# Performance work log

Measured on AMD Instinct MI355X. Metric: run time of the kernel, lower is better.

Reference implementation:

```python
import jax, jax.numpy as jnp
import numpy as np

# Config constants (from DeepSeekConfig / init_kwargs)
NUM_EXPERTS = 6
VAR_EXPERTS = 4
FIXED_EXPERTS = NUM_EXPERTS - VAR_EXPERTS  # 2
TOP_K = 2
D_MODEL = 1024
D_FF = 4 * D_MODEL
LN_EPS = 1e-5


def setup_inputs() -> dict:
    key = jax.random.key(0)
    ks = jax.random.split(key, 6)
    B, S = 2, 2048
    x = jax.random.normal(ks[0], (B, S, D_MODEL), dtype=jnp.float32)
    router_W = jax.random.normal(ks[1], (D_MODEL, VAR_EXPERTS), dtype=jnp.float32) * 0.02
    # stacked expert FFN params: (E, D, 4D) and (E, 4D, D)
    W1 = jax.random.normal(ks[2], (NUM_EXPERTS, D_MODEL, D_FF), dtype=jnp.float32) * 0.02
    b1 = jnp.zeros((NUM_EXPERTS, D_FF), dtype=jnp.float32)
    W2 = jax.random.normal(ks[3], (NUM_EXPERTS, D_FF, D_MODEL), dtype=jnp.float32) * 0.02
    b2 = jnp.zeros((NUM_EXPERTS, D_MODEL), dtype=jnp.float32)
    ln_gamma = jnp.ones((D_MODEL,), dtype=jnp.float32)
    ln_beta = jnp.zeros((D_MODEL,), dtype=jnp.float32)
    return {"x": x, "router_W": router_W, "W1": W1, "b1": b1, "W2": W2,
            "b2": b2, "ln_gamma": ln_gamma, "ln_beta": ln_beta}


def reference(x, router_W, W1, b1, W2, b2, ln_gamma, ln_beta):
    B, S, D = x.shape
    # router over the VARIABLE experts only
    router_logits = jnp.einsum('bsd,de->bse', x, router_W)          # (B,S,VAR)
    router_probs = jax.nn.softmax(router_logits, axis=-1)
    _, topk_idx = jax.lax.top_k(router_probs, TOP_K)                 # (B,S,K)
    adj_idx = topk_idx + FIXED_EXPERTS                               # global expert ids in [FIXED, NUM)

    # dense per-expert FFN on all tokens: experts[e](x) = gelu(x@W1[e]+b1[e]) @ W2[e] + b2[e]
    h = jnp.einsum('bsd,edf->ebsf', x, W1) + b1[:, None, None, :]    # (E,B,S,4D)
    h = jax.nn.gelu(h, approximate=False)                            # torch F.gelu default = exact
    all_out = jnp.einsum('ebsf,efd->ebsd', h, W2) + b2[:, None, None, :]  # (E,B,S,D)

    # fixed experts: all of experts[0:FIXED] applied to every token
    fixed_sum = all_out[:FIXED_EXPERTS].sum(axis=0)                  # (B,S,D)

    # variable experts: per-token gather of the top-k selected experts
    b_ix = jnp.arange(B)[:, None, None]
    s_ix = jnp.arange(S)[None, :, None]
    var = all_out[adj_idx, b_ix, s_ix, :]                            # (B,S,K,D)

    # cat along expert slot dim then mean == sum / (FIXED + K); topk probs unused (plain mean)
    combined = (fixed_sum + var.sum(axis=2)) / (FIXED_EXPERTS + TOP_K)

    # LayerNorm (biased variance, eps=1e-5)
    mu = combined.mean(axis=-1, keepdims=True)
    v = combined.var(axis=-1, keepdims=True)
    out = (combined - mu) / jnp.sqrt(v + LN_EPS) * ln_gamma + ln_beta
    return out, router_logits
```

## Files before the change

kernel.cpp:

```cpp
#include <hip/hip_runtime.h>
#include <cstdint>
#include <cstddef>

#define D_MODEL 1024
#define D_FF 4096
#define NTOK 4096
#define LN_EPS 1e-5f

typedef __bf16 bf16x8 __attribute__((ext_vector_type(8)));
typedef float f32x4 __attribute__((ext_vector_type(4)));
typedef unsigned short u16x4 __attribute__((ext_vector_type(4)));
typedef unsigned short u16x8 __attribute__((ext_vector_type(8)));

static __device__ __forceinline__ unsigned short f2bf(float f) {
    union { float f; unsigned u; } v; v.f = f;
    unsigned r = v.u + 0x7fffu + ((v.u >> 16) & 1u);
    return (unsigned short)(r >> 16);
}

static __device__ __forceinline__ float gelu_fast(float x) {
    float x2 = x * x;
    float a = x * __builtin_fmaf(-0.0713548162726f, x2, -1.59576912161f);
    float e = __expf(a);
    return x * __builtin_amdgcn_rcpf(1.0f + e);
}

static __device__ __forceinline__ void gload16(const void* g, void* l) {
    __builtin_amdgcn_global_load_lds(
        (const __attribute__((address_space(1))) void*)g,
        (__attribute__((address_space(3))) void*)l, 16, 0, 0);
}

static __device__ __forceinline__ void seg_of(const int* cnt, int seg[4], int pc[4]) {
    int o = 2 * NTOK;
    #pragma unroll
    for (int e = 0; e < 4; ++e) {
        int c = cnt[e * 32];
        pc[e] = (c + 127) & ~127;
        seg[e] = o;
        o += pc[e];
    }
}

__global__ __launch_bounds__(256) void convx_kernel(const float* __restrict__ x,
                                                    unsigned short* __restrict__ xb) {
    int idx = blockIdx.x * 256 + threadIdx.x;
    f32x4 v = *(const f32x4*)&x[(size_t)idx * 4];
    u16x4 b;
    b[0] = f2bf(v[0]); b[1] = f2bf(v[1]); b[2] = f2bf(v[2]); b[3] = f2bf(v[3]);
    *(u16x4*)&xb[(size_t)idx * 4] = b;
}

__global__ __launch_bounds__(256) void transpose_kernel(const float* __restrict__ W,
                                                        unsigned short* __restrict__ Wt,
                                                        int K, int N) {
    __shared__ unsigned short t[64][65];
    int k0 = blockIdx.y * 64, n0 = blockIdx.x * 64;
    const float* We = W + (size_t)blockIdx.z * K * N;
    unsigned short* Wte = Wt + (size_t)blockIdx.z * K * N;
    #pragma unroll
    for (int i = 0; i < 4; ++i) {
        int idx = threadIdx.x + i * 256;
        int kr = idx >> 4, c4 = idx & 15;
        f32x4 v = *(const f32x4*)&We[(size_t)(k0 + kr) * N + n0 + c4 * 4];
        #pragma unroll
        for (int j = 0; j < 4; ++j) t[c4 * 4 + j][kr] = f2bf(v[j]);
    }
    __syncthreads();
    #pragma unroll
    for (int i = 0; i < 2; ++i) {
        int idx = threadIdx.x + i * 256;
        int nr = idx >> 3, ck = idx & 7;
        u16x8 w;
        #pragma unroll
        for (int j = 0; j < 8; ++j) w[j] = t[nr][ck * 8 + j];
        *(u16x8*)&Wte[(size_t)(n0 + nr) * K + k0 + ck * 8] = w;
    }
}

__global__ __launch_bounds__(256) void router_kernel(
        const float* __restrict__ x, const float* __restrict__ rW,
        float* __restrict__ logits, int* __restrict__ selpk,
        int* __restrict__ slotpk, int* __restrict__ cnt, int* __restrict__ list) {
    __shared__ int se[8];
    __shared__ int sslot[8];
    int wid = threadIdx.x >> 6, lane = threadIdx.x & 63;
    int t = blockIdx.x * 4 + wid;
    const float* xr = x + (size_t)t * D_MODEL;
    float a0 = 0.f, a1 = 0.f, a2 = 0.f, a3 = 0.f;
    for (int d = lane; d < D_MODEL; d += 64) {
        float xv = xr[d];
        const float* w = rW + d * 4;
        a0 += xv * w[0]; a1 += xv * w[1]; a2 += xv * w[2]; a3 += xv * w[3];
    }
    #pragma unroll
    for (int off = 32; off; off >>= 1) {
        a0 += __shfl_xor(a0, off); a1 += __shfl_xor(a1, off);
        a2 += __shfl_xor(a2, off); a3 += __shfl_xor(a3, off);
    }
    if (lane == 0) {
        float l[4] = {a0, a1, a2, a3};
        logits[t * 4 + 0] = a0; logits[t * 4 + 1] = a1;
        logits[t * 4 + 2] = a2; logits[t * 4 + 3] = a3;
        int e0 = 0; float b = l[0];
        #pragma unroll
        for (int e = 1; e < 4; ++e) if (l[e] > b) { b = l[e]; e0 = e; }
        int e1 = -1; float b2 = -1e30f;
        #pragma unroll
        for (int e = 0; e < 4; ++e) {
            if (e == e0) continue;
            if (l[e] > b2) { b2 = l[e]; e1 = e; }
        }
        se[wid * 2] = e0; se[wid * 2 + 1] = e1;
    }
    __syncthreads();
    if (threadIdx.x == 0) {
        int cnts[4] = {0, 0, 0, 0}, base[4];
        #pragma unroll
        for (int k = 0; k < 8; ++k) cnts[se[k]]++;
        #pragma unroll
        for (int e = 0; e < 4; ++e)
            if (cnts[e]) base[e] = atomicAdd(&cnt[e * 32], cnts[e]);
        int run[4] = {0, 0, 0, 0};
        #pragma unroll
        for (int k = 0; k < 8; ++k) {
            int e = se[k];
            int s = base[e] + run[e]++;
            sslot[k] = s;
            list[e * NTOK + s] = blockIdx.x * 4 + (k >> 1);
        }
    }
    __syncthreads();
    if (lane == 0) {
        selpk[t] = se[wid * 2] | (se[wid * 2 + 1] << 8);
        slotpk[t] = sslot[wid * 2] | (sslot[wid * 2 + 1] << 16);
    }
}

__global__ __launch_bounds__(256) void pass1_kernel(
        const unsigned short* __restrict__ xb, const unsigned short* __restrict__ W1t,
        const float* __restrict__ b1, unsigned short* __restrict__ h,
        const int* __restrict__ cnt, const int* __restrict__ list, int fc, int BF) {
    __shared__ unsigned short As[128 * 64];
    __shared__ unsigned short Bs[128 * 64];
    const int e = blockIdx.z;
    const int tid = threadIdx.x, lane = tid & 63, wid = tid >> 6;
    int ecnt = NTOK, rowbase;
    if (e < 2) {
        rowbase = e * NTOK + blockIdx.y * 128;
    } else {
        int seg[4], pc[4];
        seg_of(cnt, seg, pc);
        int ev = e - 2;
        ecnt = cnt[ev * 32];
        if ((int)blockIdx.y * 128 >= pc[ev]) return;
        rowbase = seg[ev] + blockIdx.y * 128;
    }
    const int n0 = blockIdx.x * 128;

    const unsigned short* asrc[4];
    const unsigned short* bsrc[4];
    const unsigned short* W1e = W1t + (size_t)e * D_FF * D_MODEL;
    #pragma unroll
    for (int j = 0; j < 4; ++j) {
        int row = (wid * 4 + j) * 8 + (lane >> 3);
        int kc = lane & 7;
        int tok;
        if (e < 2) tok = blockIdx.y * 128 + row;
        else {
            int s = blockIdx.y * 128 + row;
            tok = (s < ecnt) ? list[(e - 2) * NTOK + s] : 0;
        }
        asrc[j] = xb + (size_t)tok * D_MODEL + ((kc ^ (row & 7)) << 3);
        bsrc[j] = W1e + (size_t)(fc + n0 + row) * D_MODEL + ((kc ^ (row & 7)) << 3);
    }
    const int wm = (wid >> 1) * 64, wn = (wid & 1) * 64;

    f32x4 acc[4][4];
    #pragma unroll
    for (int i = 0; i < 4; ++i)
        #pragma unroll
        for (int j = 0; j < 4; ++j) acc[i][j] = (f32x4)0.f;

    for (int kb = 0; kb < D_MODEL; kb += 64) {
        #pragma unroll
        for (int j = 0; j < 4; ++j) gload16(asrc[j] + kb, &As[(wid * 4 + j) * 512]);
        #pragma unroll
        for (int j = 0; j < 4; ++j) gload16(bsrc[j] + kb, &Bs[(wid * 4 + j) * 512]);
        asm volatile("s_waitcnt vmcnt(0)" ::: "memory");
        __syncthreads();
        #pragma unroll
        for (int kk = 0; kk < 2; ++kk) {
            int kof = kk * 32 + (lane >> 4) * 8;
            bf16x8 a[4], b[4];
            #pragma unroll
            for (int mi = 0; mi < 4; ++mi) {
                int r = wm + mi * 16 + (lane & 15);
                a[mi] = *(const bf16x8*)&As[r * 64 + (kof ^ ((r & 7) << 3))];
            }
            #pragma unroll
            for (int ni = 0; ni < 4; ++ni) {
                int r = wn + ni * 16 + (lane & 15);
                b[ni] = *(const bf16x8*)&Bs[r * 64 + (kof ^ ((r & 7) << 3))];
            }
            #pragma unroll
            for (int mi = 0; mi < 4; ++mi)
                #pragma unroll
                for (int ni = 0; ni < 4; ++ni)
                    acc[mi][ni] = __builtin_amdgcn_mfma_f32_16x16x32_bf16(
                        a[mi], b[ni], acc[mi][ni], 0, 0, 0);
        }
        __syncthreads();
    }

    const float* b1e = b1 + (size_t)e * D_FF + fc + n0;
    #pragma unroll
    for (int ni = 0; ni < 4; ++ni) {
        int col = wn + ni * 16 + (lane & 15);
        float bias = b1e[col];
        #pragma unroll
        for (int mi = 0; mi < 4; ++mi) {
            #pragma unroll
            for (int j = 0; j < 4; ++j) {
                int row = wm + mi * 16 + (lane >> 4) * 4 + j;
                float v = acc[mi][ni][j] + bias;
                h[(size_t)(rowbase + row) * BF + n0 + col] = f2bf(gelu_fast(v));
            }
        }
    }
}

__global__ __launch_bounds__(256) void pass2_kernel(
        const unsigned short* __restrict__ h, const unsigned short* __restrict__ W2t,
        const float* __restrict__ b2, float* __restrict__ oslab,
        const int* __restrict__ cnt, int fc, int BF, int first) {
    __shared__ unsigned short As[128 * 64];
    __shared__ unsigned short Bs[128 * 64];
    const int e = blockIdx.z;
    const int tid = threadIdx.x, lane = tid & 63, wid = tid >> 6;
    int rowbase;
    if (e < 2) {
        rowbase = e * NTOK + blockIdx.y * 128;
    } else {
        int seg[4], pc[4];
        seg_of(cnt, seg, pc);
        int ev = e - 2;
        if ((int)blockIdx.y * 128 >= pc[ev]) return;
        rowbase = seg[ev] + blockIdx.y * 128;
    }
    const int n0 = blockIdx.x * 128;

    const unsigned short* asrc[4];
    const unsigned short* bsrc[4];
    const unsigned short* W2e = W2t + (size_t)e * D_MODEL * D_FF;
    #pragma unroll
    for (int j = 0; j < 4; ++j) {
        int row = (wid * 4 + j) * 8 + (lane >> 3);
        int kc = lane & 7;
        asrc[j] = h + (size_t)(rowbase + row) * BF + ((kc ^ (row & 7)) << 3);
        bsrc[j] = W2e + (size_t)(n0 + row) * D_FF + fc + ((kc ^ (row & 7)) << 3);
    }
    const int wm = (wid >> 1) * 64, wn = (wid & 1) * 64;

    f32x4 acc[4][4];
    #pragma unroll
    for (int i = 0; i < 4; ++i)
        #pragma unroll
        for (int j = 0; j < 4; ++j) acc[i][j] = (f32x4)0.f;

    for (int kb = 0; kb < BF; kb += 64) {
        #pragma unroll
        for (int j = 0; j < 4; ++j) gload16(asrc[j] + kb, &As[(wid * 4 + j) * 512]);
        #pragma unroll
        for (int j = 0; j < 4; ++j) gload16(bsrc[j] + kb, &Bs[(wid * 4 + j) * 512]);
        asm volatile("s_waitcnt vmcnt(0)" ::: "memory");
        __syncthreads();
        #pragma unroll
        for (int kk = 0; kk < 2; ++kk) {
            int kof = kk * 32 + (lane >> 4) * 8;
            bf16x8 a[4], b[4];
            #pragma unroll
            for (int mi = 0; mi < 4; ++mi) {
                int r = wm + mi * 16 + (lane & 15);
                a[mi] = *(const bf16x8*)&As[r * 64 + (kof ^ ((r & 7) << 3))];
            }
            #pragma unroll
            for (int ni = 0; ni < 4; ++ni) {
                int r = wn + ni * 16 + (lane & 15);
                b[ni] = *(const bf16x8*)&Bs[r * 64 + (kof ^ ((r & 7) << 3))];
            }
            #pragma unroll
            for (int mi = 0; mi < 4; ++mi)
                #pragma unroll
                for (int ni = 0; ni < 4; ++ni)
                    acc[mi][ni] = __builtin_amdgcn_mfma_f32_16x16x32_bf16(
                        a[mi], b[ni], acc[mi][ni], 0, 0, 0);
        }
        __syncthreads();
    }

    const float* b2e = b2 + (size_t)e * D_MODEL + n0;
    #pragma unroll
    for (int ni = 0; ni < 4; ++ni) {
        int col = wn + ni * 16 + (lane & 15);
        float bias = first ? b2e[col] : 0.f;
        #pragma unroll
        for (int mi = 0; mi < 4; ++mi) {
            #pragma unroll
            for (int j = 0; j < 4; ++j) {
                int row = wm + mi * 16 + (lane >> 4) * 4 + j;
                size_t idx = (size_t)(rowbase + row) * D_MODEL + n0 + col;
                float v = acc[mi][ni][j] + bias;
                if (first) oslab[idx] = v;
                else       oslab[idx] += v;
            }
        }
    }
}

__global__ __launch_bounds__(256) void pass3_kernel(
        const float* __restrict__ oslab, const int* __restrict__ selpk,
        const int* __restrict__ slotpk, const int* __restrict__ cnt,
        const float* __restrict__ gamma, const float* __restrict__ beta,
        float* __restrict__ out) {
    int t = blockIdx.x;
    int seg[4], pc[4];
    seg_of(cnt, seg, pc);
    int sp = selpk[t], sl = slotpk[t];
    int e0 = sp & 0xff, e1 = (sp >> 8) & 0xff;
    int s0 = sl & 0xffff, s1 = (sl >> 16) & 0xffff;
    const float* p0 = oslab + (size_t)t * D_MODEL;
    const float* p1 = oslab + (size_t)(NTOK + t) * D_MODEL;
    const float* p2 = oslab + (size_t)(seg[e0] + s0) * D_MODEL;
    const float* p3 = oslab + (size_t)(seg[e1] + s1) * D_MODEL;
    float c[4];
    float sum = 0.f, sq = 0.f;
    #pragma unroll
    for (int i = 0; i < 4; ++i) {
        int d = threadIdx.x + i * 256;
        float v = (p0[d] + p1[d] + p2[d] + p3[d]) * 0.25f;
        c[i] = v; sum += v; sq += v * v;
    }
    #pragma unroll
    for (int off = 32; off; off >>= 1) {
        sum += __shfl_xor(sum, off);
        sq  += __shfl_xor(sq, off);
    }
    __shared__ float red[8];
    int lane = threadIdx.x & 63, wid = threadIdx.x >> 6;
    if (lane == 0) { red[wid] = sum; red[4 + wid] = sq; }
    __syncthreads();
    sum = red[0] + red[1] + red[2] + red[3];
    sq  = red[4] + red[5] + red[6] + red[7];
    float mean = sum * (1.0f / 1024.0f);
    float var = sq * (1.0f / 1024.0f) - mean * mean;
    float inv = rsqrtf(var + LN_EPS);
    #pragma unroll
    for (int i = 0; i < 4; ++i) {
        int d = threadIdx.x + i * 256;
        out[(size_t)t * D_MODEL + d] = (c[i] - mean) * inv * gamma[d] + beta[d];
    }
}

extern "C" void kernel_launch(void* const* d_in, const int* in_sizes, int n_in,
                              void* d_out, int out_size, void* d_ws, size_t ws_size,
                              hipStream_t stream) {
    const float* x   = (const float*)d_in[0];
    const float* rW  = (const float*)d_in[1];
    const float* W1  = (const float*)d_in[2];
    const float* b1  = (const float*)d_in[3];
    const float* W2  = (const float*)d_in[4];
    const float* b2  = (const float*)d_in[5];
    const float* gam = (const float*)d_in[6];
    const float* bet = (const float*)d_in[7];
    float* out = (float*)d_out;
    float* logits = out + (size_t)NTOK * D_MODEL;

    char* ws = (char*)d_ws;
    int* cnt    = (int*)ws;
    int* selpk  = (int*)(ws + 0x1000);
    int* slotpk = (int*)(ws + 0x6000);
    int* list   = (int*)(ws + 0xB000);
    unsigned short* xb  = (unsigned short*)(ws + 0x20000);
    unsigned short* W1t = (unsigned short*)(ws + 0x820000);
    unsigned short* W2t = (unsigned short*)(ws + 0x3820000);
    float* oslab        = (float*)(ws + 0x6820000);
    const size_t h_off  = 0x6820000 + (size_t)16896 * D_MODEL * 4;
    unsigned short* h   = (unsigned short*)(ws + h_off);

    int BF = 1024;
    for (int cand = 4096; cand >= 1024; cand >>= 1) {
        size_t need = h_off + (size_t)16896 * cand * 2;
        if (need <= ws_size) { BF = cand; break; }
    }

    convx_kernel<<<NTOK * D_MODEL / 4 / 256, 256, 0, stream>>>(x, xb);
    transpose_kernel<<<dim3(D_FF / 64, D_MODEL / 64, 6), 256, 0, stream>>>(W1, W1t, D_MODEL, D_FF);
    transpose_kernel<<<dim3(D_MODEL / 64, D_FF / 64, 6), 256, 0, stream>>>(W2, W2t, D_FF, D_MODEL);
    hipMemsetAsync(cnt, 0, 512, stream);
    router_kernel<<<NTOK / 4, 256, 0, stream>>>(x, rW, logits, selpk, slotpk, cnt, list);

    int nch = D_FF / BF;
    for (int c = 0; c < nch; ++c) {
        pass1_kernel<<<dim3(BF / 128, 32, 6), 256, 0, stream>>>(
            xb, W1t, b1, h, cnt, list, c * BF, BF);
        pass2_kernel<<<dim3(D_MODEL / 128, 32, 6), 256, 0, stream>>>(
            h, W2t, b2, oslab, cnt, c * BF, BF, c == 0);
    }
    pass3_kernel<<<NTOK, 256, 0, stream>>>(oslab, selpk, slotpk, cnt, gam, bet, out);
}
```

Measured before the change: 548.4 us.

## Replace pass1/pass2 GEMMs with 256x256 double-buffered 8-wave GEMM kernel

```diff
diff --git a/kernel.cpp b/kernel.cpp
--- a/kernel.cpp
+++ b/kernel.cpp
@@ -6,6 +6,7 @@
 #define D_FF 4096
 #define NTOK 4096
 #define LN_EPS 1e-5f
+#define SLAB_ROWS 17408
 
 typedef __bf16 bf16x8 __attribute__((ext_vector_type(8)));
 typedef float f32x4 __attribute__((ext_vector_type(4)));
@@ -16,6 +17,11 @@
     union { float f; unsigned u; } v; v.f = f;
     unsigned r = v.u + 0x7fffu + ((v.u >> 16) & 1u);
     return (unsigned short)(r >> 16);
+}
+
+static __device__ __forceinline__ float b2f(unsigned short u) {
+    union { unsigned u; float f; } v; v.u = (unsigned)u << 16;
+    return v.f;
 }
 
 static __device__ __forceinline__ float gelu_fast(float x) {
@@ -36,7 +42,7 @@
     #pragma unroll
     for (int e = 0; e < 4; ++e) {
         int c = cnt[e * 32];
-        pc[e] = (c + 127) & ~127;
+        pc[e] = (c + 255) & ~255;
         seg[e] = o;
         o += pc[e];
     }
@@ -137,189 +143,135 @@
     }
 }
 
-__global__ __launch_bounds__(256) void pass1_kernel(
-        const unsigned short* __restrict__ xb, const unsigned short* __restrict__ W1t,
-        const float* __restrict__ b1, unsigned short* __restrict__ h,
-        const int* __restrict__ cnt, const int* __restrict__ list, int fc, int BF) {
-    __shared__ unsigned short As[128 * 64];
-    __shared__ unsigned short Bs[128 * 64];
+template<int GELU>
+__global__ __launch_bounds__(512, 2) void gemm8_kernel(
+        const unsigned short* __restrict__ A, const unsigned short* __restrict__ B,
+        const float* __restrict__ bias, int bias_stride, int ldo,
+        unsigned short* __restrict__ out,
+        const int* __restrict__ cnt, const int* __restrict__ list, int K) {
+    __shared__ unsigned short lds[2][2][256 * 64];
     const int e = blockIdx.z;
-    const int tid = threadIdx.x, lane = tid & 63, wid = tid >> 6;
-    int ecnt = NTOK, rowbase;
+    const int tid = threadIdx.x, l = tid & 63, w = tid >> 6;
+    int rowbase;
+    int ecnt = NTOK;
     if (e < 2) {
-        rowbase = e * NTOK + blockIdx.y * 128;
+        rowbase = e * NTOK + blockIdx.y * 256;
     } else {
         int seg[4], pc[4];
         seg_of(cnt, seg, pc);
         int ev = e - 2;
         ecnt = cnt[ev * 32];
-        if ((int)blockIdx.y * 128 >= pc[ev]) return;
-        rowbase = seg[ev] + blockIdx.y * 128;
-    }
-    const int n0 = blockIdx.x * 128;
+        if ((int)blockIdx.y * 256 >= pc[ev]) return;
+        rowbase = seg[ev] + blockIdx.y * 256;
+    }
+    const int n0 = blockIdx.x * 256;
+    const unsigned short* Be = B + (size_t)e * (4096 * 1024);
 
     const unsigned short* asrc[4];
     const unsigned short* bsrc[4];
-    const unsigned short* W1e = W1t + (size_t)e * D_FF * D_MODEL;
-    #pragma unroll
-    for (int j = 0; j < 4; ++j) {
-        int row = (wid * 4 + j) * 8 + (lane >> 3);
-        int kc = lane & 7;
-        int tok;
-        if (e < 2) tok = blockIdx.y * 128 + row;
-        else {
-            int s = blockIdx.y * 128 + row;
-            tok = (s < ecnt) ? list[(e - 2) * NTOK + s] : 0;
-        }
-        asrc[j] = xb + (size_t)tok * D_MODEL + ((kc ^ (row & 7)) << 3);
-        bsrc[j] = W1e + (size_t)(fc + n0 + row) * D_MODEL + ((kc ^ (row & 7)) << 3);
-    }
-    const int wm = (wid >> 1) * 64, wn = (wid & 1) * 64;
-
-    f32x4 acc[4][4];
-    #pragma unroll
-    for (int i = 0; i < 4; ++i)
+    #pragma unroll
+    for (int i = 0; i < 4; ++i) {
+        int row = i * 64 + w * 8 + (l >> 3);
+        int piece = ((l & 7) ^ (row & 7)) << 3;
+        size_t arow;
+        if (GELU) {
+            int s = blockIdx.y * 256 + row;
+            if (e < 2) arow = (size_t)s;
+            else       arow = (size_t)((s < ecnt) ? list[(e - 2) * NTOK + s] : 0);
+        } else {
+            arow = (size_t)(rowbase + row);
+        }
+        asrc[i] = A + arow * K + piece;
+        bsrc[i] = Be + (size_t)(n0 + row) * K + piece;
+    }
+
+    const int wr = w >> 2, wc = w & 3;
+    const int rl = l & 15, kq = l >> 4;
+
+    float bv[4];
+    #pragma unroll
+    for (int ni = 0; ni < 4; ++ni)
+        bv[ni] = bias[(size_t)e * bias_stride + n0 + wc * 64 + ni * 16 + rl];
+
+    f32x4 acc[8][4];
+    #pragma unroll
+    for (int i = 0; i < 8; ++i)
         #pragma unroll
         for (int j = 0; j < 4; ++j) acc[i][j] = (f32x4)0.f;
 
-    for (int kb = 0; kb < D_MODEL; kb += 64) {
-        #pragma unroll
-        for (int j = 0; j < 4; ++j) gload16(asrc[j] + kb, &As[(wid * 4 + j) * 512]);
-        #pragma unroll
-        for (int j = 0; j < 4; ++j) gload16(bsrc[j] + kb, &Bs[(wid * 4 + j) * 512]);
-        asm volatile("s_waitcnt vmcnt(0)" ::: "memory");
-        __syncthreads();
+    const int nt = K / 64;
+
+    #define STAGE(bf, t)                                                        \
+        {                                                                       \
+            unsigned short* la = &lds[bf][0][(w * 8) * 64];                     \
+            unsigned short* lb = &lds[bf][1][(w * 8) * 64];                     \
+            _Pragma("unroll")                                                   \
+            for (int i = 0; i < 4; ++i) {                                       \
+                gload16(asrc[i] + (t) * 64, la + i * 4096);                     \
+                gload16(bsrc[i] + (t) * 64, lb + i * 4096);                     \
+            }                                                                   \
+        }
+
+    STAGE(0, 0);
+    STAGE(1, 1);
+
+    for (int t = 0; t < nt; ++t) {
+        const int cur = t & 1;
+        if (t < nt - 1) { asm volatile("s_waitcnt vmcnt(8)" ::: "memory"); }
+        else            { asm volatile("s_waitcnt vmcnt(0)" ::: "memory"); }
+        __builtin_amdgcn_s_barrier();
+        const unsigned short* LA = &lds[cur][0][0];
+        const unsigned short* LB = &lds[cur][1][0];
         #pragma unroll
         for (int kk = 0; kk < 2; ++kk) {
-            int kof = kk * 32 + (lane >> 4) * 8;
-            bf16x8 a[4], b[4];
+            bf16x8 bfr[4];
             #pragma unroll
-            for (int mi = 0; mi < 4; ++mi) {
-                int r = wm + mi * 16 + (lane & 15);
-                a[mi] = *(const bf16x8*)&As[r * 64 + (kof ^ ((r & 7) << 3))];
+            for (int ni = 0; ni < 4; ++ni) {
+                int n = wc * 64 + ni * 16 + rl;
+                bfr[ni] = *(const bf16x8*)&LB[n * 64 + (((kk * 4 + kq) ^ (n & 7)) << 3)];
             }
             #pragma unroll
-            for (int ni = 0; ni < 4; ++ni) {
-                int r = wn + ni * 16 + (lane & 15);
-                b[ni] = *(const bf16x8*)&Bs[r * 64 + (kof ^ ((r & 7) << 3))];
+            for (int mh = 0; mh < 2; ++mh) {
+                bf16x8 afr[4];
+                #pragma unroll
+                for (int i = 0; i < 4; ++i) {
+                    int r = wr * 128 + (mh * 4 + i) * 16 + rl;
+                    afr[i] = *(const bf16x8*)&LA[r * 64 + (((kk * 4 + kq) ^ (r & 7)) << 3)];
+                }
+                __builtin_amdgcn_s_barrier();
+                __builtin_amdgcn_s_setprio(1);
+                #pragma unroll
+                for (int i = 0; i < 4; ++i)
+                    #pragma unroll
+                    for (int ni = 0; ni < 4; ++ni)
+                        acc[mh * 4 + i][ni] = __builtin_amdgcn_mfma_f32_16x16x32_bf16(
+                            afr[i], bfr[ni], acc[mh * 4 + i][ni], 0, 0, 0);
+                __builtin_amdgcn_s_setprio(0);
+                __builtin_amdgcn_s_barrier();
             }
-            #pragma unroll
-            for (int mi = 0; mi < 4; ++mi)
-                #pragma unroll
-                for (int ni = 0; ni < 4; ++ni)
-                    acc[mi][ni] = __builtin_amdgcn_mfma_f32_16x16x32_bf16(
-                        a[mi], b[ni], acc[mi][ni], 0, 0, 0);
-        }
-        __syncthreads();
-    }
-
-    const float* b1e = b1 + (size_t)e * D_FF + fc + n0;
+        }
+        if (t + 2 < nt) STAGE(cur, t + 2);
+    }
+    #undef STAGE
+
     #pragma unroll
     for (int ni = 0; ni < 4; ++ni) {
-        int col = wn + ni * 16 + (lane & 15);
-        float bias = b1e[col];
-        #pragma unroll
-        for (int mi = 0; mi < 4; ++mi) {
+        int c = n0 + wc * 64 + ni * 16 + rl;
+        #pragma unroll
+        for (int mi = 0; mi < 8; ++mi) {
             #pragma unroll
             for (int j = 0; j < 4; ++j) {
-                int row = wm + mi * 16 + (lane >> 4) * 4 + j;
-                float v = acc[mi][ni][j] + bias;
-                h[(size_t)(rowbase + row) * BF + n0 + col] = f2bf(gelu_fast(v));
+                int r = wr * 128 + mi * 16 + kq * 4 + j;
+                float v = acc[mi][ni][j] + bv[ni];
+                if (GELU) v = gelu_fast(v);
+                out[(size_t)(rowbase + r) * ldo + c] = f2bf(v);
             }
         }
     }
 }
 
-__global__ __launch_bounds__(256) void pass2_kernel(
-        const unsigned short* __restrict__ h, const unsigned short* __restrict__ W2t,
-        const float* __restrict__ b2, float* __restrict__ oslab,
-        const int* __restrict__ cnt, int fc, int BF, int first) {
-    __shared__ unsigned short As[128 * 64];
-    __shared__ unsigned short Bs[128 * 64];
-    const int e = blockIdx.z;
-    const int tid = threadIdx.x, lane = tid & 63, wid = tid >> 6;
-    int rowbase;
-    if (e < 2) {
-        rowbase = e * NTOK + blockIdx.y * 128;
-    } else {
-        int seg[4], pc[4];
-        seg_of(cnt, seg, pc);
-        int ev = e - 2;
-        if ((int)blockIdx.y * 128 >= pc[ev]) return;
-        rowbase = seg[ev] + blockIdx.y * 128;
-    }
-    const int n0 = blockIdx.x * 128;
-
-    const unsigned short* asrc[4];
-    const unsigned short* bsrc[4];
-    const unsigned short* W2e = W2t + (size_t)e * D_MODEL * D_FF;
-    #pragma unroll
-    for (int j = 0; j < 4; ++j) {
-        int row = (wid * 4 + j) * 8 + (lane >> 3);
-        int kc = lane & 7;
-        asrc[j] = h + (size_t)(rowbase + row) * BF + ((kc ^ (row & 7)) << 3);
-        bsrc[j] = W2e + (size_t)(n0 + row) * D_FF + fc + ((kc ^ (row & 7)) << 3);
-    }
-    const int wm = (wid >> 1) * 64, wn = (wid & 1) * 64;
-
-    f32x4 acc[4][4];
-    #pragma unroll
-    for (int i = 0; i < 4; ++i)
-        #pragma unroll
-        for (int j = 0; j < 4; ++j) acc[i][j] = (f32x4)0.f;
-
-    for (int kb = 0; kb < BF; kb += 64) {
-        #pragma unroll
-        for (int j = 0; j < 4; ++j) gload16(asrc[j] + kb, &As[(wid * 4 + j) * 512]);
-        #pragma unroll
-        for (int j = 0; j < 4; ++j) gload16(bsrc[j] + kb, &Bs[(wid * 4 + j) * 512]);
-        asm volatile("s_waitcnt vmcnt(0)" ::: "memory");
-        __syncthreads();
-        #pragma unroll
-        for (int kk = 0; kk < 2; ++kk) {
-            int kof = kk * 32 + (lane >> 4) * 8;
-            bf16x8 a[4], b[4];
-            #pragma unroll
-            for (int mi = 0; mi < 4; ++mi) {
-                int r = wm + mi * 16 + (lane & 15);
-                a[mi] = *(const bf16x8*)&As[r * 64 + (kof ^ ((r & 7) << 3))];
-            }
-            #pragma unroll
-            for (int ni = 0; ni < 4; ++ni) {
-                int r = wn + ni * 16 + (lane & 15);
-                b[ni] = *(const bf16x8*)&Bs[r * 64 + (kof ^ ((r & 7) << 3))];
-            }
-            #pragma unroll
-            for (int mi = 0; mi < 4; ++mi)
-                #pragma unroll
-                for (int ni = 0; ni < 4; ++ni)
-                    acc[mi][ni] = __builtin_amdgcn_mfma_f32_16x16x32_bf16(
-                        a[mi], b[ni], acc[mi][ni], 0, 0, 0);
-        }
-        __syncthreads();
-    }
-
-    const float* b2e = b2 + (size_t)e * D_MODEL + n0;
-    #pragma unroll
-    for (int ni = 0; ni < 4; ++ni) {
-        int col = wn + ni * 16 + (lane & 15);
-        float bias = first ? b2e[col] : 0.f;
-        #pragma unroll
-        for (int mi = 0; mi < 4; ++mi) {
-            #pragma unroll
-            for (int j = 0; j < 4; ++j) {
-                int row = wm + mi * 16 + (lane >> 4) * 4 + j;
-                size_t idx = (size_t)(rowbase + row) * D_MODEL + n0 + col;
-                float v = acc[mi][ni][j] + bias;
-                if (first) oslab[idx] = v;
-                else       oslab[idx] += v;
-            }
-        }
-    }
-}
-
 __global__ __launch_bounds__(256) void pass3_kernel(
-        const float* __restrict__ oslab, const int* __restrict__ selpk,
+        const unsigned short* __restrict__ oslab, const int* __restrict__ selpk,
         const int* __restrict__ slotpk, const int* __restrict__ cnt,
         const float* __restrict__ gamma, const float* __restrict__ beta,
         float* __restrict__ out) {
@@ -329,16 +281,16 @@
     int sp = selpk[t], sl = slotpk[t];
     int e0 = sp & 0xff, e1 = (sp >> 8) & 0xff;
     int s0 = sl & 0xffff, s1 = (sl >> 16) & 0xffff;
-    const float* p0 = oslab + (size_t)t * D_MODEL;
-    const float* p1 = oslab + (size_t)(NTOK + t) * D_MODEL;
-    const float* p2 = oslab + (size_t)(seg[e0] + s0) * D_MODEL;
-    const float* p3 = oslab + (size_t)(seg[e1] + s1) * D_MODEL;
+    const unsigned short* p0 = oslab + (size_t)t * D_MODEL;
+    const unsigned short* p1 = oslab + (size_t)(NTOK + t) * D_MODEL;
+    const unsigned short* p2 = oslab + (size_t)(seg[e0] + s0) * D_MODEL;
+    const unsigned short* p3 = oslab + (size_t)(seg[e1] + s1) * D_MODEL;
     float c[4];
     float sum = 0.f, sq = 0.f;
     #pragma unroll
     for (int i = 0; i < 4; ++i) {
         int d = threadIdx.x + i * 256;
-        float v = (p0[d] + p1[d] + p2[d] + p3[d]) * 0.25f;
+        float v = (b2f(p0[d]) + b2f(p1[d]) + b2f(p2[d]) + b2f(p3[d])) * 0.25f;
         c[i] = v; sum += v; sq += v * v;
     }
     #pragma unroll
@@ -381,18 +333,11 @@
     int* selpk  = (int*)(ws + 0x1000);
     int* slotpk = (int*)(ws + 0x6000);
     int* list   = (int*)(ws + 0xB000);
-    unsigned short* xb  = (unsigned short*)(ws + 0x20000);
-    unsigned short* W1t = (unsigned short*)(ws + 0x820000);
-    unsigned short* W2t = (unsigned short*)(ws + 0x3820000);
-    float* oslab        = (float*)(ws + 0x6820000);
-    const size_t h_off  = 0x6820000 + (size_t)16896 * D_MODEL * 4;
-    unsigned short* h   = (unsigned short*)(ws + h_off);
-
-    int BF = 1024;
-    for (int cand = 4096; cand >= 1024; cand >>= 1) {
-        size_t need = h_off + (size_t)16896 * cand * 2;
-        if (need <= ws_size) { BF = cand; break; }
-    }
+    unsigned short* xb    = (unsigned short*)(ws + 0x20000);
+    unsigned short* W1t   = (unsigned short*)(ws + 0x820000);
+    unsigned short* W2t   = (unsigned short*)(ws + 0x3820000);
+    unsigned short* oslab = (unsigned short*)(ws + 0x6820000);
+    unsigned short* h     = (unsigned short*)(ws + 0x8A20000);
 
     convx_kernel<<<NTOK * D_MODEL / 4 / 256, 256, 0, stream>>>(x, xb);
     transpose_kernel<<<dim3(D_FF / 64, D_MODEL / 64, 6), 256, 0, stream>>>(W1, W1t, D_MODEL, D_FF);
@@ -400,12 +345,10 @@
     hipMemsetAsync(cnt, 0, 512, stream);
     router_kernel<<<NTOK / 4, 256, 0, stream>>>(x, rW, logits, selpk, slotpk, cnt, list);
 
-    int nch = D_FF / BF;
-    for (int c = 0; c < nch; ++c) {
-        pass1_kernel<<<dim3(BF / 128, 32, 6), 256, 0, stream>>>(
-            xb, W1t, b1, h, cnt, list, c * BF, BF);
-        pass2_kernel<<<dim3(D_MODEL / 128, 32, 6), 256, 0, stream>>>(
-            h, W2t, b2, oslab, cnt, c * BF, BF, c == 0);
-    }
+    gemm8_kernel<1><<<dim3(D_FF / 256, 16, 6), 512, 0, stream>>>(
+        xb, W1t, b1, D_FF, D_FF, h, cnt, list, D_MODEL);
+    gemm8_kernel<0><<<dim3(D_MODEL / 256, 16, 6), 512, 0, stream>>>(
+        h, W2t, b2, D_MODEL, D_MODEL, oslab, cnt, list, D_FF);
+
     pass3_kernel<<<NTOK, 256, 0, stream>>>(oslab, selpk, slotpk, cnt, gam, bet, out);
 }
```

Result: no change. 548.2 us (-0.0%).
